# Kernel optimization log

Measured on AMD Instinct MI355X. Metric: run time of the kernel, lower is better.

## Reference

```python
import jax, jax.numpy as jnp
import numpy as np

B, T, D = 8, 1, 4096          # batch, fresh tokens (single-token decode), d_model
H, HD, KV = 32, 128, 512      # n_heads, head_dim, mla_kv_lrank
PAST = 8191                   # cached compressed-KV length
SCALE = HD ** -0.5


def setup_inputs() -> dict:
    key = jax.random.key(0)
    ks = jax.random.split(key, 6)
    return {
        "x": jax.random.normal(ks[0], (B, T, D), dtype=jnp.float32),
        "past_c": jax.random.normal(ks[1], (B, PAST, KV), dtype=jnp.float32),
        # absorbed q*k_up projection: [H, D, KV]
        "absorbed_qk": jax.random.normal(ks[2], (H, D, KV), dtype=jnp.float32) * 0.02,
        # _compress_kv: Linear(D -> KV)
        "w_compress": jax.random.normal(ks[3], (D, KV), dtype=jnp.float32) * 0.02,
        # v_up: Linear(KV -> H*HD)
        "w_v": jax.random.normal(ks[4], (KV, H * HD), dtype=jnp.float32) * 0.02,
        # out_proj: Linear(H*HD -> D)
        "w_o": jax.random.normal(ks[5], (H * HD, D), dtype=jnp.float32) * 0.02,
    }


def reference(x, past_c, absorbed_qk, w_compress, w_v, w_o):
    b, t, d = x.shape
    # compress fresh tokens and extend the compressed KV cache
    c = x @ w_compress                                 # [B, T, KV]
    c_full = jnp.concatenate([past_c, c], axis=1)      # [B, total, KV]
    total = c_full.shape[1]

    # absorbed query projection: Q_abs = x @ absorbed_qk per head
    q_abs = jnp.einsum('btd,hdk->bhtk', x, absorbed_qk)        # [B, H, T, KV]
    # attention scores directly against compressed cache
    scores = jnp.einsum('bhtk,bsk->bhts', q_abs, c_full) * SCALE  # [B, H, T, total]

    # causal mask: query t (absolute pos total-T+t) sees kv pos p iff p <= total-T+t
    q_pos = jnp.arange(t)[:, None] + (total - t)       # [T, 1]
    kv_pos = jnp.arange(total)[None, :]                # [1, total]
    causal = q_pos >= kv_pos                           # [T, total]
    scores = jnp.where(causal[None, None], scores, -jnp.inf)
    attn = jax.nn.softmax(scores, axis=-1)             # [B, H, T, total]

    # up-project V from compressed cache
    v = (c_full @ w_v).reshape(b, total, H, HD)        # [B, total, H, HD]
    out = jnp.einsum('bhts,bshd->bthd', attn, v).reshape(b, t, H * HD)
    return out @ w_o                                   # [B, T, D]
```

## Files before the change

### kernel.cpp

```cpp
#include <hip/hip_runtime.h>
#include <stdint.h>

#define B_ 8
#define D_ 4096
#define H_ 32
#define HD_ 128
#define KV_ 512
#define PAST_ 8191
#define SCALE_ 0.08838834764831845f

#define OFF_QP   0u
#define OFF_CP   8388608u
#define OFF_QABS 8650752u
#define OFF_CNEW 8781824u
#define OFF_ML   8785920u
#define OFF_CTXP 8818688u
#define OFF_CTX2 17207296u

typedef float f32x4 __attribute__((ext_vector_type(4)));
typedef float f32x2 __attribute__((ext_vector_type(2)));
typedef short s16x8 __attribute__((ext_vector_type(8)));
typedef short s16x4 __attribute__((ext_vector_type(4)));

__device__ __forceinline__ unsigned short f2bf(float f) {
    unsigned u = __float_as_uint(f);
    u = (u + 0x7FFFu + ((u >> 16) & 1u)) >> 16;
    return (unsigned short)u;
}
__device__ __forceinline__ float bf2f(unsigned short s) {
    return __uint_as_float(((unsigned)s) << 16);
}

__global__ __launch_bounds__(128) void k_qabs(const float* __restrict__ x,
                                              const float* __restrict__ aqk,
                                              const float* __restrict__ wc,
                                              float* __restrict__ ws) {
    const int h = blockIdx.x;
    const int dc = blockIdx.y;
    const int t = threadIdx.x;
    alignas(16) __shared__ float xT[64][8];
    {
        const int b = t >> 4, g = t & 15;
        const f32x4 v = *(const f32x4*)(x + (size_t)b * D_ + dc * 64 + g * 4);
#pragma unroll
        for (int e = 0; e < 4; ++e) xT[g * 4 + e][b] = v[e];
    }
    __syncthreads();
    const float* A = ((h < H_) ? (aqk + (size_t)h * D_ * KV_) : wc)
                   + ((size_t)dc * 64) * KV_ + t * 4;

    f32x4 acc[B_];
#pragma unroll
    for (int b = 0; b < B_; ++b) acc[b] = (f32x4){0.f, 0.f, 0.f, 0.f};

    for (int r0 = 0; r0 < 64; r0 += 16) {
        f32x4 a[16];
#pragma unroll
        for (int u = 0; u < 16; ++u)
            a[u] = *(const f32x4*)(A + (size_t)(r0 + u) * KV_);
#pragma unroll
        for (int u = 0; u < 16; ++u) {
            const f32x4 xa = *(const f32x4*)&xT[r0 + u][0];
            const f32x4 xb = *(const f32x4*)&xT[r0 + u][4];
            acc[0] += xa[0] * a[u];
            acc[1] += xa[1] * a[u];
            acc[2] += xa[2] * a[u];
            acc[3] += xa[3] * a[u];
            acc[4] += xb[0] * a[u];
            acc[5] += xb[1] * a[u];
            acc[6] += xb[2] * a[u];
            acc[7] += xb[3] * a[u];
        }
    }
#pragma unroll
    for (int b = 0; b < B_; ++b) {
        float* dst = (h < H_)
            ? (ws + OFF_QP + (size_t)dc * 131072u + (size_t)(b * H_ + h) * KV_ + t * 4)
            : (ws + OFF_CP + (size_t)dc * 4096u + (size_t)b * KV_ + t * 4);
        *(f32x4*)dst = acc[b];
    }
}

__global__ __launch_bounds__(512) void k_qred(float* __restrict__ ws) {
    const int bx = blockIdx.x;
    const int t = threadIdx.x;
    const int pg = t >> 8, tt = t & 255;
    alignas(16) __shared__ float part[2][512];

    const float* src;
    size_t stride;
    float* dst;
    if (bx < 256) {
        src = ws + OFF_QP + (size_t)pg * 32u * 131072u + (size_t)bx * KV_ + 2 * tt;
        stride = 131072u;
        dst = ws + OFF_QABS + (size_t)bx * KV_;
    } else {
        const int b = bx - 256;
        src = ws + OFF_CP + (size_t)pg * 32u * 4096u + (size_t)b * KV_ + 2 * tt;
        stride = 4096u;
        dst = ws + OFF_CNEW + (size_t)b * KV_;
    }
    f32x2 s = {0.f, 0.f};
#pragma unroll 8
    for (int p = 0; p < 32; ++p) {
        const f32x2 v = *(const f32x2*)(src + (size_t)p * stride);
        s[0] += v[0]; s[1] += v[1];
    }
    *(f32x2*)&part[pg][2 * tt] = s;
    __syncthreads();
    if (t < 256) {
        const f32x2 p0 = *(const f32x2*)&part[0][2 * t];
        const f32x2 p1 = *(const f32x2*)&part[1][2 * t];
        *(f32x2*)(dst + 2 * t) = (f32x2){p0[0] + p1[0], p0[1] + p1[1]};
    }
}

__global__ __launch_bounds__(256, 2) void k_attn(const float* __restrict__ past_c,
                                                 float* __restrict__ ws) {
    const int bx = blockIdx.x;
    const int b = bx >> 6, sc = bx & 63;
    const int t = threadIdx.x;
    const int w = t >> 6, lane = t & 63, quad = lane >> 4, ln = lane & 15;
    const int ni = w & 1, kh = w >> 1;

    alignas(16) __shared__ unsigned short ch[16 * 520];
    alignas(16) __shared__ unsigned short cl[16 * 520];
    alignas(16) __shared__ unsigned short cT[512 * 20];
    alignas(16) __shared__ float Sp[2 * 16 * 33];
    alignas(16) __shared__ unsigned short P[32 * 20];
    __shared__ float alpha[32];

    s16x8 qh[8], ql[8];
    {
        const float* qp = ws + OFF_QABS + (size_t)(b * H_ + ni * 16 + ln) * KV_ + kh * 256 + quad * 8;
#pragma unroll
        for (int st = 0; st < 8; ++st) {
            const f32x4 v0 = *(const f32x4*)(qp + st * 32);
            const f32x4 v1 = *(const f32x4*)(qp + st * 32 + 4);
#pragma unroll
            for (int i = 0; i < 8; ++i) {
                const float xv = ((i < 4) ? v0[i] : v1[i - 4]) * SCALE_;
                const unsigned short hi = f2bf(xv);
                qh[st][i] = (short)hi;
                ql[st][i] = (short)f2bf(xv - bf2f(hi));
            }
        }
    }

    f32x4 cacc[16];
#pragma unroll
    for (int i = 0; i < 16; ++i) cacc[i] = (f32x4){0.f, 0.f, 0.f, 0.f};
    float m_run = -1e30f, l_run = 0.f;

    for (int sub = 0; sub < 8; ++sub) {
        const int s0 = sc * 128 + sub * 16;
        {
            const int r = t >> 4, m = t & 15;
            const int sg = s0 + r;
            const float* src = (sg == PAST_) ? (ws + OFF_CNEW + (size_t)b * KV_)
                                             : (past_c + ((size_t)b * PAST_ + sg) * KV_);
#pragma unroll
            for (int i = 0; i < 8; ++i) {
                const int k = m * 4 + i * 64;
                const f32x4 v = *(const f32x4*)(src + k);
                s16x4 hi4, lo4;
#pragma unroll
                for (int e = 0; e < 4; ++e) {
                    const unsigned short hh = f2bf(v[e]);
                    hi4[e] = (short)hh;
                    lo4[e] = (short)f2bf(v[e] - bf2f(hh));
                    const int kk = k + e;
                    cT[kk * 20 + (r ^ ((((kk) >> 4) & 3) << 2))] = hh;
                }
                *(s16x4*)&ch[r * 520 + k] = hi4;
                *(s16x4*)&cl[r * 520 + k] = lo4;
            }
        }
        __syncthreads();
        {
            f32x4 sacc = {0.f, 0.f, 0.f, 0.f};
#pragma unroll
            for (int st = 0; st < 8; ++st) {
                const int ko = kh * 256 + st * 32 + quad * 8;
                const s16x8 ah = *(const s16x8*)&ch[ln * 520 + ko];
                const s16x8 al = *(const s16x8*)&cl[ln * 520 + ko];
                sacc = __builtin_amdgcn_mfma_f32_16x16x32_bf16(ah, qh[st], sacc, 0, 0, 0);
                sacc = __builtin_amdgcn_mfma_f32_16x16x32_bf16(ah, ql[st], sacc, 0, 0, 0);
                sacc = __builtin_amdgcn_mfma_f32_16x16x32_bf16(al, qh[st], sacc, 0, 0, 0);
            }
#pragma unroll
            for (int r = 0; r < 4; ++r)
                Sp[kh * 528 + (quad * 4 + r) * 33 + ni * 16 + ln] = sacc[r];
        }
        __syncthreads();
        if (t < 32) {
            const int h = t;
            float sv[16];
            float msub = -1e30f;
#pragma unroll
            for (int s = 0; s < 16; ++s) {
                sv[s] = Sp[s * 33 + h] + Sp[528 + s * 33 + h];
                msub = fmaxf(msub, sv[s]);
            }
            const float m_new = fmaxf(m_run, msub);
            const float al_ = __expf(m_run - m_new);
            float lsum = 0.f;
#pragma unroll
            for (int s = 0; s < 16; s += 2) {
                const float p0 = __expf(sv[s] - m_new);
                const float p1 = __expf(sv[s + 1] - m_new);
                lsum += p0 + p1;
                const unsigned pk = (unsigned)f2bf(p0) | ((unsigned)f2bf(p1) << 16);
                *(unsigned*)&P[h * 20 + s] = pk;
            }
            l_run = l_run * al_ + lsum;
            m_run = m_new;
            alpha[h] = al_;
        }
        __syncthreads();
        {
            const float av = alpha[ni * 16 + ln];
            const s16x4 bp = *(const s16x4*)&P[(ni * 16 + ln) * 20 + quad * 4];
#pragma unroll
            for (int ti = 0; ti < 16; ++ti) {
                const int krow = (kh * 16 + ti) * 16 + ln;
                const int sg2 = (quad ^ ((krow >> 4) & 3)) << 2;
                const s16x4 ac = *(const s16x4*)&cT[krow * 20 + sg2];
                f32x4 cc = cacc[ti];
                cc[0] *= av; cc[1] *= av; cc[2] *= av; cc[3] *= av;
                cacc[ti] = __builtin_amdgcn_mfma_f32_16x16x16bf16_1k(ac, bp, cc, 0, 0, 0);
            }
        }
        __syncthreads();
    }
    {
        float* cp = ws + OFF_CTXP + ((size_t)(b * 64 + sc) * H_ + (ni * 16 + ln)) * KV_;
#pragma unroll
        for (int ti = 0; ti < 16; ++ti) {
            const int k0 = (kh * 16 + ti) * 16 + quad * 4;
            *(f32x4*)(cp + k0) = cacc[ti];
        }
    }
    if (t < 32) {
        float* mp = ws + OFF_ML + (size_t)(b * 64 + sc) * 64;
        mp[t] = m_run;
        mp[32 + t] = l_run;
    }
}

__global__ __launch_bounds__(512) void k_cv(const float* __restrict__ wv,
                                            float* __restrict__ ws) {
    const int b = blockIdx.x >> 5, h = blockIdx.x & 31;
    const int t = threadIdx.x;
    __shared__ float ml[64], ll[64], wgt[64];
    alignas(16) __shared__ float cx[512];
    alignas(16) __shared__ float cpart[2][512];
    alignas(16) __shared__ float red[16][128];
    if (t < 64) {
        const float* mp = ws + OFF_ML + (size_t)(b * 64 + t) * 64;
        ml[t] = mp[h];
        ll[t] = mp[32 + h];
    }
    __syncthreads();
    float M = -1e30f;
    for (int s = 0; s < 64; ++s) M = fmaxf(M, ml[s]);
    if (t < 64) wgt[t] = __expf(ml[t] - M);
    __syncthreads();
    float L = 0.f;
    for (int s = 0; s < 64; ++s) L += ll[s] * wgt[s];
    const float invL = 1.f / L;
    const int half = t >> 8, tt = t & 255;
    f32x2 acc = {0.f, 0.f};
#pragma unroll 8
    for (int s = half; s < 64; s += 2) {
        const float f = wgt[s];
        const f32x2 v = *(const f32x2*)(ws + OFF_CTXP + ((size_t)(b * 64 + s) * H_ + h) * KV_ + 2 * tt);
        acc[0] += f * v[0];
        acc[1] += f * v[1];
    }
    *(f32x2*)&cpart[half][2 * tt] = acc;
    __syncthreads();
    if (t < 256) {
        const f32x2 p0 = *(const f32x2*)&cpart[0][2 * t];
        const f32x2 p1 = *(const f32x2*)&cpart[1][2 * t];
        *(f32x2*)&cx[2 * t] = (f32x2){(p0[0] + p1[0]) * invL, (p0[1] + p1[1]) * invL};
    }
    __syncthreads();
    const int r = t >> 5, c = (t & 31) * 4;
    f32x4 a4 = {0.f, 0.f, 0.f, 0.f};
#pragma unroll 4
    for (int kb = 0; kb < 32; ++kb) {
        const int k = kb * 16 + r;
        const f32x4 w4 = *(const f32x4*)(wv + (size_t)k * (H_ * HD_) + h * HD_ + c);
        a4 += cx[k] * w4;
    }
    *(f32x4*)&red[r][c] = a4;
    __syncthreads();
    if (t < 128) {
        float s = 0.f;
#pragma unroll
        for (int rr = 0; rr < 16; ++rr) s += red[rr][t];
        ws[OFF_CTX2 + (size_t)b * D_ + h * HD_ + t] = s;
    }
}

__global__ __launch_bounds__(256) void k_out(const float* __restrict__ wo,
                                             const float* __restrict__ ws,
                                             float* __restrict__ out) {
    const int dc = blockIdx.x, jc = blockIdx.y;
    const int t = threadIdx.x;
    alignas(16) __shared__ float c2[B_][256];
#pragma unroll
    for (int i = 0; i < 8; ++i) {
        const int e = t + i * 256;
        const int bb = e >> 8, jj = e & 255;
        c2[bb][jj] = ws[OFF_CTX2 + (size_t)bb * D_ + jc * 256 + jj];
    }
    __syncthreads();
    const int d = dc * 256 + t;
    float acc[B_] = {};
    for (int j = 0; j < 256; j += 8) {
        float wreg[8];
#pragma unroll
        for (int u = 0; u < 8; ++u)
            wreg[u] = wo[(size_t)(jc * 256 + j + u) * D_ + d];
#pragma unroll
        for (int b = 0; b < B_; ++b) {
            const f32x4 c0 = *(const f32x4*)&c2[b][j];
            const f32x4 c1 = *(const f32x4*)&c2[b][j + 4];
            acc[b] += c0[0] * wreg[0] + c0[1] * wreg[1] + c0[2] * wreg[2] + c0[3] * wreg[3]
                    + c1[0] * wreg[4] + c1[1] * wreg[5] + c1[2] * wreg[6] + c1[3] * wreg[7];
        }
    }
#pragma unroll
    for (int b = 0; b < B_; ++b)
        atomicAdd(&out[b * D_ + d], acc[b]);
}

extern "C" void kernel_launch(void* const* d_in, const int* in_sizes, int n_in,
                              void* d_out, int out_size, void* d_ws, size_t ws_size,
                              hipStream_t stream) {
    const float* x      = (const float*)d_in[0];
    const float* past_c = (const float*)d_in[1];
    const float* aqk    = (const float*)d_in[2];
    const float* wc     = (const float*)d_in[3];
    const float* wv     = (const float*)d_in[4];
    const float* wo     = (const float*)d_in[5];
    float* out = (float*)d_out;
    float* ws  = (float*)d_ws;

    hipMemsetAsync(d_out, 0, (size_t)out_size * sizeof(float), stream);

    k_qabs<<<dim3(33, 64), 128, 0, stream>>>(x, aqk, wc, ws);
    k_qred<<<dim3(264), 512, 0, stream>>>(ws);
    k_attn<<<dim3(512), 256, 0, stream>>>(past_c, ws);
    k_cv<<<dim3(256), 512, 0, stream>>>(wv, ws);
    k_out<<<dim3(16, 16), 256, 0, stream>>>(wo, ws, out);
}
```

Before: 561.7 us.

## Prefetch next KV sub-tile in registers and enlarge qabs D-chunks

The attention kernel now loads the next 16-row slice of the compressed cache into registers right after the barrier, so global loads overlap the MFMA score computation instead of stalling at the top of each sub-iteration. Separately, the absorbed-query kernel handles 256 D rows per block instead of 64, cutting the grid fourfold and the partial-sum buffer and reduction work from 32 partials to 8. This raises register pressure in the attention kernel, which is launched with 2 blocks per CU, and reduces the number of blocks available to the qabs kernel.

```diff
diff --git a/kernel.cpp b/kernel.cpp
--- a/kernel.cpp
+++ b/kernel.cpp
@@ -10,12 +10,12 @@
 #define SCALE_ 0.08838834764831845f
 
 #define OFF_QP   0u
-#define OFF_CP   8388608u
-#define OFF_QABS 8650752u
-#define OFF_CNEW 8781824u
-#define OFF_ML   8785920u
-#define OFF_CTXP 8818688u
-#define OFF_CTX2 17207296u
+#define OFF_CP   2097152u
+#define OFF_QABS 2162688u
+#define OFF_CNEW 2293760u
+#define OFF_ML   2297856u
+#define OFF_CTXP 2330624u
+#define OFF_CTX2 10719232u
 
 typedef float f32x4 __attribute__((ext_vector_type(4)));
 typedef float f32x2 __attribute__((ext_vector_type(2)));
@@ -38,22 +38,24 @@
     const int h = blockIdx.x;
     const int dc = blockIdx.y;
     const int t = threadIdx.x;
-    alignas(16) __shared__ float xT[64][8];
-    {
-        const int b = t >> 4, g = t & 15;
-        const f32x4 v = *(const f32x4*)(x + (size_t)b * D_ + dc * 64 + g * 4);
+    alignas(16) __shared__ float xT[256][8];
+#pragma unroll
+    for (int j = 0; j < 4; ++j) {
+        const int i = t + j * 128;
+        const int b = i >> 6, g = i & 63;
+        const f32x4 v = *(const f32x4*)(x + (size_t)b * D_ + dc * 256 + g * 4);
 #pragma unroll
         for (int e = 0; e < 4; ++e) xT[g * 4 + e][b] = v[e];
     }
     __syncthreads();
     const float* A = ((h < H_) ? (aqk + (size_t)h * D_ * KV_) : wc)
-                   + ((size_t)dc * 64) * KV_ + t * 4;
+                   + ((size_t)dc * 256) * KV_ + t * 4;
 
     f32x4 acc[B_];
 #pragma unroll
     for (int b = 0; b < B_; ++b) acc[b] = (f32x4){0.f, 0.f, 0.f, 0.f};
 
-    for (int r0 = 0; r0 < 64; r0 += 16) {
+    for (int r0 = 0; r0 < 256; r0 += 16) {
         f32x4 a[16];
 #pragma unroll
         for (int u = 0; u < 16; ++u)
@@ -91,18 +93,18 @@
     size_t stride;
     float* dst;
     if (bx < 256) {
-        src = ws + OFF_QP + (size_t)pg * 32u * 131072u + (size_t)bx * KV_ + 2 * tt;
+        src = ws + OFF_QP + (size_t)pg * 8u * 131072u + (size_t)bx * KV_ + 2 * tt;
         stride = 131072u;
         dst = ws + OFF_QABS + (size_t)bx * KV_;
     } else {
         const int b = bx - 256;
-        src = ws + OFF_CP + (size_t)pg * 32u * 4096u + (size_t)b * KV_ + 2 * tt;
+        src = ws + OFF_CP + (size_t)pg * 8u * 4096u + (size_t)b * KV_ + 2 * tt;
         stride = 4096u;
         dst = ws + OFF_CNEW + (size_t)b * KV_;
     }
     f32x2 s = {0.f, 0.f};
-#pragma unroll 8
-    for (int p = 0; p < 32; ++p) {
+#pragma unroll
+    for (int p = 0; p < 8; ++p) {
         const f32x2 v = *(const f32x2*)(src + (size_t)p * stride);
         s[0] += v[0]; s[1] += v[1];
     }
@@ -152,17 +154,24 @@
     for (int i = 0; i < 16; ++i) cacc[i] = (f32x4){0.f, 0.f, 0.f, 0.f};
     float m_run = -1e30f, l_run = 0.f;
 
+    const int r_st = t >> 4, m_st = t & 15;
+
+    f32x4 pre[8];
+    {
+        const int sg = sc * 128 + r_st;
+        const float* src = (sg == PAST_) ? (ws + OFF_CNEW + (size_t)b * KV_)
+                                         : (past_c + ((size_t)b * PAST_ + sg) * KV_);
+#pragma unroll
+        for (int i = 0; i < 8; ++i)
+            pre[i] = *(const f32x4*)(src + m_st * 4 + i * 64);
+    }
+
     for (int sub = 0; sub < 8; ++sub) {
-        const int s0 = sc * 128 + sub * 16;
         {
-            const int r = t >> 4, m = t & 15;
-            const int sg = s0 + r;
-            const float* src = (sg == PAST_) ? (ws + OFF_CNEW + (size_t)b * KV_)
-                                             : (past_c + ((size_t)b * PAST_ + sg) * KV_);
 #pragma unroll
             for (int i = 0; i < 8; ++i) {
-                const int k = m * 4 + i * 64;
-                const f32x4 v = *(const f32x4*)(src + k);
+                const int k = m_st * 4 + i * 64;
+                const f32x4 v = pre[i];
                 s16x4 hi4, lo4;
 #pragma unroll
                 for (int e = 0; e < 4; ++e) {
@@ -170,13 +179,21 @@
                     hi4[e] = (short)hh;
                     lo4[e] = (short)f2bf(v[e] - bf2f(hh));
                     const int kk = k + e;
-                    cT[kk * 20 + (r ^ ((((kk) >> 4) & 3) << 2))] = hh;
+                    cT[kk * 20 + (r_st ^ ((((kk) >> 4) & 3) << 2))] = hh;
                 }
-                *(s16x4*)&ch[r * 520 + k] = hi4;
-                *(s16x4*)&cl[r * 520 + k] = lo4;
+                *(s16x4*)&ch[r_st * 520 + k] = hi4;
+                *(s16x4*)&cl[r_st * 520 + k] = lo4;
             }
         }
         __syncthreads();
+        if (sub < 7) {
+            const int sg = sc * 128 + (sub + 1) * 16 + r_st;
+            const float* src = (sg == PAST_) ? (ws + OFF_CNEW + (size_t)b * KV_)
+                                             : (past_c + ((size_t)b * PAST_ + sg) * KV_);
+#pragma unroll
+            for (int i = 0; i < 8; ++i)
+                pre[i] = *(const f32x4*)(src + m_st * 4 + i * 64);
+        }
         {
             f32x4 sacc = {0.f, 0.f, 0.f, 0.f};
 #pragma unroll
@@ -351,7 +368,7 @@
 
     hipMemsetAsync(d_out, 0, (size_t)out_size * sizeof(float), stream);
 
-    k_qabs<<<dim3(33, 64), 128, 0, stream>>>(x, aqk, wc, ws);
+    k_qabs<<<dim3(33, 16), 128, 0, stream>>>(x, aqk, wc, ws);
     k_qred<<<dim3(264), 512, 0, stream>>>(ws);
     k_attn<<<dim3(512), 256, 0, stream>>>(past_c, ws);
     k_cv<<<dim3(256), 512, 0, stream>>>(wv, ws);
```

Result: faster. 545.4 us (-2.9%).
